# Optimization experiments

Measured on AMD Instinct MI355X. Metric: run time of the kernel, lower is better.

## Reference

```python
import jax, jax.numpy as jnp
import numpy as np

C = 32           # max_channels (in == out == 32, stride 1)
K = 3            # base kernel size
EXP_NITER = 5    # ConvExponential iterations -> effective kernel 11x11
POWER_IT = 3     # FantasticFour power iterations
B, H, W = 16, 256, 256


def _l2n(x):
    # L2Normalize over all dims (applied on store via right_inverse and again on read; idempotent)
    return x / (jnp.sqrt(jnp.sum(x * x)) + 1e-12)


def _skew(k):
    # K - flip(K^T, spatial)
    return k - jnp.flip(jnp.transpose(k, (1, 0, 2, 3)), axis=(2, 3))


def _fantastic_four(kernel, u1, u2, u3, u4):
    u1, u2, u3, u4 = map(_l2n, (u1, u2, u3, u4))
    for _ in range(POWER_IT):
        v1 = _l2n(jnp.sum(kernel * u1, axis=(1, 3), keepdims=True))
        u1 = _l2n(jnp.sum(kernel * v1, axis=(0, 2), keepdims=True))
        v2 = _l2n(jnp.sum(kernel * u2, axis=(1, 2), keepdims=True))
        u2 = _l2n(jnp.sum(kernel * v2, axis=(0, 3), keepdims=True))
        v3 = _l2n(jnp.sum(kernel * u3, axis=(1, 2, 3), keepdims=True))
        u3 = _l2n(jnp.sum(kernel * v3, axis=0, keepdims=True))
        v4 = _l2n(jnp.sum(kernel * u4, axis=(0, 2, 3), keepdims=True))
        u4 = _l2n(jnp.sum(kernel * v4, axis=1, keepdims=True))
    sg = jax.lax.stop_gradient  # sigmas use detached u/v, grad only via kernel
    s1 = jnp.sum(kernel * sg(u1) * sg(v1))
    s2 = jnp.sum(kernel * sg(u2) * sg(v2))
    s3 = jnp.sum(kernel * sg(u3) * sg(v3))
    s4 = jnp.sum(kernel * sg(u4) * sg(v4))
    sigma = jnp.minimum(jnp.minimum(s1, s2), jnp.minimum(s3, s4))
    return kernel / sigma


def _conv_exp(kernel):
    # kernel_global = I + K + K*K/2! + ... (kernel composition = full spatial convolution)
    p = (K - 1) // 2
    ident = jnp.pad(jnp.eye(C, dtype=kernel.dtype)[:, :, None, None],
                    ((0, 0), (0, 0), (p, p), (p, p)))
    kg = kernel + ident            # (C, C, K, K)
    ki = kernel
    rhs = jnp.flip(kernel, axis=(2, 3))  # flip -> lax correlation becomes full convolution
    for i in range(2, EXP_NITER + 1):
        # out[o,d,y,x] = sum_{c,p,q} ki[c,d,y-p,x-q] * kernel[o,c,p,q]
        inp = jnp.transpose(ki, (1, 0, 2, 3))  # (d, c, h, w) as NCHW
        out = jax.lax.conv_general_dilated(
            inp, rhs, window_strides=(1, 1),
            padding=[(K - 1, K - 1), (K - 1, K - 1)],
            dimension_numbers=('NCHW', 'OIHW', 'NCHW'))
        ki = jnp.transpose(out, (1, 0, 2, 3)) / float(i)
        kg = jnp.pad(kg, ((0, 0), (0, 0), (p, p), (p, p))) + ki
    return kg  # (C, C, 11, 11) for K=3, EXP_NITER=5


def reference(x, weight_raw, bias, u1, u2, u3, u4):
    w = _conv_exp(_fantastic_four(_skew(weight_raw), u1, u2, u3, u4))
    pad = w.shape[2] // 2  # 5
    z = jnp.pad(x, ((0, 0), (0, 0), (pad, pad), (pad, pad)), mode='wrap')  # circular
    z = jax.lax.conv_general_dilated(
        z, w, window_strides=(1, 1), padding='VALID',
        dimension_numbers=('NCHW', 'OIHW', 'NCHW'))
    return z + bias[None, :, None, None]


def setup_inputs() -> dict:
    key = jax.random.key(0)
    ks = jax.random.split(key, 7)
    return {
        'x': jax.random.normal(ks[0], (B, C, H, W), dtype=jnp.float32),
        'weight_raw': jax.random.normal(ks[1], (C, C, K, K), dtype=jnp.float32),
        'bias': jax.random.normal(ks[2], (C,), dtype=jnp.float32),
        'u1': jax.random.normal(ks[3], (1, C, 1, K), dtype=jnp.float32),
        'u2': jax.random.normal(ks[4], (1, C, K, 1), dtype=jnp.float32),
        'u3': jax.random.normal(ks[5], (1, C, K, K), dtype=jnp.float32),
        'u4': jax.random.normal(ks[6], (C, 1, K, K), dtype=jnp.float32),
    }
```

## Files before the change

kernel.cpp:

```cpp
#include <hip/hip_runtime.h>
#include <math.h>

typedef __bf16 bf16x8 __attribute__((ext_vector_type(8)));
typedef float f32x16 __attribute__((ext_vector_type(16)));
typedef unsigned int uint4v __attribute__((ext_vector_type(4)));

__device__ __forceinline__ unsigned short bf16_rne(float f) {
    unsigned u = __float_as_uint(f);
    unsigned r = u + 0x7fffu + ((u >> 16) & 1u);
    return (unsigned short)(r >> 16);
}
__device__ __forceinline__ float bf16_to_f(unsigned short h) {
    return __uint_as_float(((unsigned)h) << 16);
}

__device__ __forceinline__ float block_sum256(float v, float* red) {
    #pragma unroll
    for (int off = 32; off > 0; off >>= 1)
        v += __shfl_down(v, off, 64);
    const int tid = threadIdx.x;
    if ((tid & 63) == 0) red[tid >> 6] = v;
    __syncthreads();
    float tot = red[0] + red[1] + red[2] + red[3];
    __syncthreads();
    return tot;
}

__device__ __forceinline__ void l2n_lds(float* a, int n, float* red) {
    float s = 0.f;
    for (int i = threadIdx.x; i < n; i += 256) s += a[i] * a[i];
    const float tot = block_sum256(s, red);
    const float sc = 1.0f / (sqrtf(tot) + 1e-12f);
    for (int i = threadIdx.x; i < n; i += 256) a[i] *= sc;
    __syncthreads();
}

__global__ __launch_bounds__(256) void ff_kernel(
    const float* __restrict__ wr,
    const float* __restrict__ u1g, const float* __restrict__ u2g,
    const float* __restrict__ u3g, const float* __restrict__ u4g,
    float* __restrict__ kf_out)
{
    __shared__ float ks[9216];
    __shared__ float u1[96], v1[96], u2[96], v2[96];
    __shared__ float u3[288], u4[288], v3[32], v4[32];
    __shared__ float red[8];
    const int tid = threadIdx.x;

    for (int i = tid; i < 9216; i += 256) {
        int q  = i % 3;
        int p  = (i / 3) % 3;
        int ic = (i / 9) % 32;
        int oc = i / 288;
        ks[i] = wr[i] - wr[ic * 288 + oc * 9 + (2 - p) * 3 + (2 - q)];
    }
    if (tid < 96) { u1[tid] = u1g[tid]; u2[tid] = u2g[tid]; }
    for (int i = tid; i < 288; i += 256) { u3[i] = u3g[i]; u4[i] = u4g[i]; }
    __syncthreads();
    l2n_lds(u1, 96, red);
    l2n_lds(u2, 96, red);
    l2n_lds(u3, 288, red);
    l2n_lds(u4, 288, red);

    for (int it = 0; it < 3; ++it) {
        if (tid < 96) {
            int o = tid / 3, p = tid % 3;
            float s = 0.f;
            for (int i = 0; i < 32; ++i)
                for (int q = 0; q < 3; ++q)
                    s += ks[o * 288 + i * 9 + p * 3 + q] * u1[i * 3 + q];
            v1[tid] = s;
        }
        __syncthreads();
        l2n_lds(v1, 96, red);
        if (tid < 96) {
            int i = tid / 3, q = tid % 3;
            float s = 0.f;
            for (int o = 0; o < 32; ++o)
                for (int p = 0; p < 3; ++p)
                    s += ks[o * 288 + i * 9 + p * 3 + q] * v1[o * 3 + p];
            u1[tid] = s;
        }
        __syncthreads();
        l2n_lds(u1, 96, red);
        if (tid < 96) {
            int o = tid / 3, q = tid % 3;
            float s = 0.f;
            for (int i = 0; i < 32; ++i)
                for (int p = 0; p < 3; ++p)
                    s += ks[o * 288 + i * 9 + p * 3 + q] * u2[i * 3 + p];
            v2[tid] = s;
        }
        __syncthreads();
        l2n_lds(v2, 96, red);
        if (tid < 96) {
            int i = tid / 3, p = tid % 3;
            float s = 0.f;
            for (int o = 0; o < 32; ++o)
                for (int q = 0; q < 3; ++q)
                    s += ks[o * 288 + i * 9 + p * 3 + q] * v2[o * 3 + q];
            u2[tid] = s;
        }
        __syncthreads();
        l2n_lds(u2, 96, red);
        if (tid < 32) {
            float s = 0.f;
            for (int i = 0; i < 32; ++i)
                for (int pq = 0; pq < 9; ++pq)
                    s += ks[tid * 288 + i * 9 + pq] * u3[i * 9 + pq];
            v3[tid] = s;
        }
        __syncthreads();
        l2n_lds(v3, 32, red);
        for (int j = tid; j < 288; j += 256) {
            float s = 0.f;
            for (int o = 0; o < 32; ++o)
                s += ks[o * 288 + j] * v3[o];
            u3[j] = s;
        }
        __syncthreads();
        l2n_lds(u3, 288, red);
        if (tid < 32) {
            float s = 0.f;
            for (int o = 0; o < 32; ++o)
                for (int pq = 0; pq < 9; ++pq)
                    s += ks[o * 288 + tid * 9 + pq] * u4[o * 9 + pq];
            v4[tid] = s;
        }
        __syncthreads();
        l2n_lds(v4, 32, red);
        for (int j = tid; j < 288; j += 256) {
            int o = j / 9, pq = j - o * 9;
            float s = 0.f;
            for (int i = 0; i < 32; ++i)
                s += ks[o * 288 + i * 9 + pq] * v4[i];
            u4[j] = s;
        }
        __syncthreads();
        l2n_lds(u4, 288, red);
    }

    float p1 = 0.f, p2 = 0.f, p3 = 0.f, p4 = 0.f;
    for (int idx = tid; idx < 9216; idx += 256) {
        int q = idx % 3;
        int p = (idx / 3) % 3;
        int i = (idx / 9) % 32;
        int o = idx / 288;
        float k = ks[idx];
        p1 += k * u1[i * 3 + q] * v1[o * 3 + p];
        p2 += k * u2[i * 3 + p] * v2[o * 3 + q];
        p3 += k * u3[i * 9 + p * 3 + q] * v3[o];
        p4 += k * u4[o * 9 + p * 3 + q] * v4[i];
    }
    float s1 = block_sum256(p1, red);
    float s2 = block_sum256(p2, red);
    float s3 = block_sum256(p3, red);
    float s4 = block_sum256(p4, red);
    float sigma = fminf(fminf(s1, s2), fminf(s3, s4));
    for (int idx = tid; idx < 9216; idx += 256)
        kf_out[idx] = ks[idx] / sigma;
}

__global__ void initacc_kernel(const float* __restrict__ kf, float* __restrict__ wacc) {
    int idx = blockIdx.x * 256 + threadIdx.x;
    if (idx >= 123904) return;
    int o = idx / 3872;
    int rem = idx - o * 3872;
    int c = rem / 121;
    int yx = rem - c * 121;
    int y = yx / 11, x = yx - y * 11;
    float v = (o == c && y == 5 && x == 5) ? 1.0f : 0.0f;
    if (y >= 4 && y <= 6 && x >= 4 && x <= 6)
        v += kf[o * 288 + c * 9 + (y - 4) * 3 + (x - 4)];
    wacc[idx] = v;
}

__global__ void expstep_kernel(const float* __restrict__ kf, const float* __restrict__ ki,
                               float* __restrict__ ko, float* __restrict__ wacc,
                               int S, float scale)
{
    const int S2 = S + 2;
    const int off = (11 - S2) >> 1;
    const int o = blockIdx.x >> 5;
    const int d = blockIdx.x & 31;
    for (int yx = threadIdx.x; yx < S2 * S2; yx += blockDim.x) {
        int y = yx / S2, xx = yx - y * S2;
        float s = 0.f;
        for (int c = 0; c < 32; ++c) {
            const float* kfo = kf + o * 288 + c * 9;
            const float* kic = ki + (c * 32 + d) * S * S;
            #pragma unroll
            for (int p = 0; p < 3; ++p) {
                int yy = y - p;
                if (yy < 0 || yy >= S) continue;
                #pragma unroll
                for (int q = 0; q < 3; ++q) {
                    int xq = xx - q;
                    if (xq < 0 || xq >= S) continue;
                    s += kfo[p * 3 + q] * kic[yy * S + xq];
                }
            }
        }
        s *= scale;
        ko[(o * 32 + d) * S2 * S2 + yx] = s;
        wacc[(o * 32 + d) * 121 + (y + off) * 11 + (xx + off)] += s;
    }
}

__global__ void wprep_kernel(const float* __restrict__ wacc, uint4v* __restrict__ wbuf) {
    int idx = blockIdx.x * 256 + threadIdx.x;
    if (idx >= 30976) return;
    int lane  = idx & 63;
    int split = (idx >> 6) & 1;
    int ch    = (idx >> 7) & 1;
    int tap   = idx >> 8;
    int o     = lane & 31;
    int cbase = ch * 16 + ((lane >> 5) << 3);
    unsigned short v[8];
    #pragma unroll
    for (int j = 0; j < 8; ++j) {
        float w = wacc[o * 3872 + (cbase + j) * 121 + tap];
        unsigned short h = bf16_rne(w);
        v[j] = split ? bf16_rne(w - bf16_to_f(h)) : h;
    }
    uint4v u;
    u.x = (unsigned)v[0] | ((unsigned)v[1] << 16);
    u.y = (unsigned)v[2] | ((unsigned)v[3] << 16);
    u.z = (unsigned)v[4] | ((unsigned)v[5] << 16);
    u.w = (unsigned)v[6] | ((unsigned)v[7] << 16);
    wbuf[idx] = u;
}

__device__ __forceinline__ void pack2(unsigned short* dst, const unsigned short* v) {
    uint4v u;
    u.x = (unsigned)v[0] | ((unsigned)v[1] << 16);
    u.y = (unsigned)v[2] | ((unsigned)v[3] << 16);
    u.z = (unsigned)v[4] | ((unsigned)v[5] << 16);
    u.w = (unsigned)v[6] | ((unsigned)v[7] << 16);
    *(uint4v*)dst = u;
}

template<bool TWOPASS, bool DOSTAGE, bool STHI>
__device__ __forceinline__ void mfma_phase(
    f32x16 (&acc)[4],
    const uint4v* __restrict__ wbuf,
    const uint4v* __restrict__ pb,
    unsigned short* __restrict__ dst,
    int schlf,
    int chlf,
    const float* __restrict__ x,
    int b, int Y0, int X0, int tid, int lane, int ywave, int myoff)
{
    const int wb0 = chlf * 128 + lane;
    #pragma unroll 1
    for (int q = 0; q < 11; ++q) {
        if (DOSTAGE) {
            if (!(q & 1) && (q >> 1) < 5) {
                int pix = tid + ((q >> 1) << 8);
                if (pix < 1092) {
                    int rr = pix / 42, ss = pix - rr * 42;
                    int gy = (Y0 + rr - 5) & 255;
                    int gx = (X0 + ss - 5) & 255;
                    const float* xp = x + (((size_t)(b * 32 + schlf * 16)) << 16)
                                        + (gy << 8) + gx;
                    unsigned short wv[16];
                    #pragma unroll
                    for (int cc = 0; cc < 16; ++cc) {
                        float v = xp[(size_t)cc << 16];
                        unsigned short h = bf16_rne(v);
                        wv[cc] = STHI ? h : bf16_rne(v - bf16_to_f(h));
                    }
                    pack2(&dst[pix * 8], wv);
                    pack2(&dst[(1092 + pix) * 8], wv + 8);
                }
            }
        }
        uint4v ah[8], al[8];
        ah[0] = wbuf[wb0 + q * 256];
        ah[1] = wbuf[wb0 + (11 + q) * 256];
        ah[2] = wbuf[wb0 + (22 + q) * 256];
        if (TWOPASS) {
            al[0] = wbuf[wb0 + q * 256 + 64];
            al[1] = wbuf[wb0 + (11 + q) * 256 + 64];
            al[2] = wbuf[wb0 + (22 + q) * 256 + 64];
        }
        bf16x8 B = __builtin_bit_cast(bf16x8, pb[ywave * 42 + q + myoff]);
        #pragma unroll
        for (int r = 0; r < 14; ++r) {
            const bf16x8 cB = B;
            if (r < 13)
                B = __builtin_bit_cast(bf16x8, pb[(ywave + r + 1) * 42 + q + myoff]);
            if (r + 3 <= 10) {
                ah[(r + 3) & 7] = wbuf[wb0 + ((r + 3) * 11 + q) * 256];
                if (TWOPASS)
                    al[(r + 3) & 7] = wbuf[wb0 + ((r + 3) * 11 + q) * 256 + 64];
            }
            const int plo = (r - 3 > 0) ? r - 3 : 0;
            const int phi = (r < 10) ? r : 10;
            __builtin_amdgcn_s_setprio(1);
            #pragma unroll
            for (int p = plo; p <= phi; ++p)
                acc[r - p] = __builtin_amdgcn_mfma_f32_32x32x16_bf16(
                    __builtin_bit_cast(bf16x8, ah[p & 7]), cB, acc[r - p], 0, 0, 0);
            if (TWOPASS) {
                #pragma unroll
                for (int p = plo; p <= phi; ++p)
                    acc[r - p] = __builtin_amdgcn_mfma_f32_32x32x16_bf16(
                        __builtin_bit_cast(bf16x8, al[p & 7]), cB, acc[r - p], 0, 0, 0);
            }
            __builtin_amdgcn_s_setprio(0);
        }
    }
}

__global__ __launch_bounds__(256, 2) void conv_mfma_kernel(
    const float* __restrict__ x, const uint4v* __restrict__ wbuf,
    const float* __restrict__ bias, float* __restrict__ out)
{
    __shared__ unsigned short bufA[2 * 1092 * 8];
    __shared__ unsigned short bufB[2 * 1092 * 8];
    __shared__ float biasS[32];

    const int b    = blockIdx.z;
    const int Y0   = blockIdx.y << 4;
    const int X0   = blockIdx.x << 5;
    const int tid  = threadIdx.x;
    const int lane = tid & 63;
    const int ywave = (tid >> 6) << 2;
    const int myoff = (lane & 31) + (lane >> 5) * 1092;

    if (tid < 32) biasS[tid] = bias[tid];

    f32x16 acc[4];
    #pragma unroll
    for (int s = 0; s < 4; ++s)
        #pragma unroll
        for (int r = 0; r < 16; ++r) acc[s][r] = 0.f;

    {
        const float* xb = x + (((size_t)(b * 32)) << 16);
        for (int pix = tid; pix < 1092; pix += 256) {
            int r = pix / 42, s = pix - r * 42;
            int gy = (Y0 + r - 5) & 255;
            int gx = (X0 + s - 5) & 255;
            const float* xp = xb + (gy << 8) + gx;
            unsigned short hv[16], lv[16];
            #pragma unroll
            for (int cc = 0; cc < 16; ++cc) {
                float v = xp[(size_t)cc << 16];
                unsigned short h = bf16_rne(v);
                hv[cc] = h;
                lv[cc] = bf16_rne(v - bf16_to_f(h));
            }
            pack2(&bufA[pix * 8], hv);
            pack2(&bufA[(1092 + pix) * 8], hv + 8);
            pack2(&bufB[pix * 8], lv);
            pack2(&bufB[(1092 + pix) * 8], lv + 8);
        }
    }
    __syncthreads();

    mfma_phase<true, false, false>(acc, wbuf, (const uint4v*)bufA, nullptr, 0, 0,
                                   x, b, Y0, X0, tid, lane, ywave, myoff);
    __syncthreads();

    mfma_phase<false, true, true>(acc, wbuf, (const uint4v*)bufB, bufA, 1, 0,
                                  x, b, Y0, X0, tid, lane, ywave, myoff);
    __syncthreads();

    mfma_phase<true, true, false>(acc, wbuf, (const uint4v*)bufA, bufB, 1, 1,
                                  x, b, Y0, X0, tid, lane, ywave, myoff);
    __syncthreads();

    mfma_phase<false, false, false>(acc, wbuf, (const uint4v*)bufB, nullptr, 1, 1,
                                    x, b, Y0, X0, tid, lane, ywave, myoff);

    const int colx = X0 + (lane & 31);
    const int half = lane >> 5;
    #pragma unroll
    for (int s = 0; s < 4; ++s) {
        int y = Y0 + ywave + s;
        #pragma unroll
        for (int r = 0; r < 16; ++r) {
            int o = (r & 3) + ((r >> 2) << 3) + (half << 2);
            out[(((size_t)(b * 32 + o)) << 16) + (y << 8) + colx] = acc[s][r] + biasS[o];
        }
    }
}

extern "C" void kernel_launch(void* const* d_in, const int* in_sizes, int n_in,
                              void* d_out, int out_size, void* d_ws, size_t ws_size,
                              hipStream_t stream) {
    const float* x    = (const float*)d_in[0];
    const float* wraw = (const float*)d_in[1];
    const float* bias = (const float*)d_in[2];
    const float* u1   = (const float*)d_in[3];
    const float* u2   = (const float*)d_in[4];
    const float* u3   = (const float*)d_in[5];
    const float* u4   = (const float*)d_in[6];
    float* out = (float*)d_out;

    float* ws   = (float*)d_ws;
    float* kf   = ws;
    float* bufA = kf + 9216;
    float* bufB = bufA + 123904;
    float* wacc = bufB + 123904;
    uint4v* wbuf = (uint4v*)(wacc + 123904);

    ff_kernel<<<1, 256, 0, stream>>>(wraw, u1, u2, u3, u4, kf);
    initacc_kernel<<<484, 256, 0, stream>>>(kf, wacc);
    expstep_kernel<<<1024, 128, 0, stream>>>(kf, kf,   bufA, wacc, 3, 0.5f);
    expstep_kernel<<<1024, 128, 0, stream>>>(kf, bufA, bufB, wacc, 5, 1.0f / 3.0f);
    expstep_kernel<<<1024, 128, 0, stream>>>(kf, bufB, bufA, wacc, 7, 0.25f);
    expstep_kernel<<<1024, 128, 0, stream>>>(kf, bufA, bufB, wacc, 9, 0.2f);
    wprep_kernel<<<121, 256, 0, stream>>>(wacc, wbuf);

    conv_mfma_kernel<<<dim3(8, 16, 16), 256, 0, stream>>>(x, wbuf, bias, out);
}
```

Baseline: 931.7 us.

## Use single shared buffer with serialized staging to raise occupancy to three blocks

Replaces the two double-buffered shared-memory planes with one buffer. Each hi/lo plane is now staged synchronously before its MFMA pass instead of being overlapped with the previous pass, and launch bounds are raised to 3 blocks per CU. Halving LDS use and capping registers is meant to let more blocks hide latency across CUs. In exchange, global loads are no longer overlapped with MFMA work inside a block, and the tighter register cap could cause spills. Staging is also fully serialized within each block.

```diff
diff --git a/kernel.cpp b/kernel.cpp
--- a/kernel.cpp
+++ b/kernel.cpp
@@ -240,41 +240,38 @@
     *(uint4v*)dst = u;
 }
 
-template<bool TWOPASS, bool DOSTAGE, bool STHI>
-__device__ __forceinline__ void mfma_phase(
+__device__ __forceinline__ void stage_plane(
+    unsigned short* __restrict__ buf, const float* __restrict__ x,
+    int b, int chlf, bool lo, int Y0, int X0, int tid)
+{
+    const float* xb = x + (((size_t)(b * 32 + chlf * 16)) << 16);
+    for (int pix = tid; pix < 1092; pix += 256) {
+        int r = pix / 42, s = pix - r * 42;
+        int gy = (Y0 + r - 5) & 255;
+        int gx = (X0 + s - 5) & 255;
+        const float* xp = xb + (gy << 8) + gx;
+        unsigned short v[16];
+        #pragma unroll
+        for (int cc = 0; cc < 16; ++cc) {
+            float t = xp[(size_t)cc << 16];
+            unsigned short h = bf16_rne(t);
+            v[cc] = lo ? bf16_rne(t - bf16_to_f(h)) : h;
+        }
+        pack2(&buf[pix * 8], v);
+        pack2(&buf[(1092 + pix) * 8], v + 8);
+    }
+}
+
+template<bool TWOPASS>
+__device__ __forceinline__ void mfma_pass(
     f32x16 (&acc)[4],
     const uint4v* __restrict__ wbuf,
     const uint4v* __restrict__ pb,
-    unsigned short* __restrict__ dst,
-    int schlf,
-    int chlf,
-    const float* __restrict__ x,
-    int b, int Y0, int X0, int tid, int lane, int ywave, int myoff)
+    int chlf, int lane, int ywave, int myoff)
 {
     const int wb0 = chlf * 128 + lane;
     #pragma unroll 1
     for (int q = 0; q < 11; ++q) {
-        if (DOSTAGE) {
-            if (!(q & 1) && (q >> 1) < 5) {
-                int pix = tid + ((q >> 1) << 8);
-                if (pix < 1092) {
-                    int rr = pix / 42, ss = pix - rr * 42;
-                    int gy = (Y0 + rr - 5) & 255;
-                    int gx = (X0 + ss - 5) & 255;
-                    const float* xp = x + (((size_t)(b * 32 + schlf * 16)) << 16)
-                                        + (gy << 8) + gx;
-                    unsigned short wv[16];
-                    #pragma unroll
-                    for (int cc = 0; cc < 16; ++cc) {
-                        float v = xp[(size_t)cc << 16];
-                        unsigned short h = bf16_rne(v);
-                        wv[cc] = STHI ? h : bf16_rne(v - bf16_to_f(h));
-                    }
-                    pack2(&dst[pix * 8], wv);
-                    pack2(&dst[(1092 + pix) * 8], wv + 8);
-                }
-            }
-        }
         uint4v ah[8], al[8];
         ah[0] = wbuf[wb0 + q * 256];
         ah[1] = wbuf[wb0 + (11 + q) * 256];
@@ -313,12 +310,11 @@
     }
 }
 
-__global__ __launch_bounds__(256, 2) void conv_mfma_kernel(
+__global__ __launch_bounds__(256, 3) void conv_mfma_kernel(
     const float* __restrict__ x, const uint4v* __restrict__ wbuf,
     const float* __restrict__ bias, float* __restrict__ out)
 {
-    __shared__ unsigned short bufA[2 * 1092 * 8];
-    __shared__ unsigned short bufB[2 * 1092 * 8];
+    __shared__ unsigned short sbuf[2 * 1092 * 8];
     __shared__ float biasS[32];
 
     const int b    = blockIdx.z;
@@ -337,43 +333,19 @@
         #pragma unroll
         for (int r = 0; r < 16; ++r) acc[s][r] = 0.f;
 
-    {
-        const float* xb = x + (((size_t)(b * 32)) << 16);
-        for (int pix = tid; pix < 1092; pix += 256) {
-            int r = pix / 42, s = pix - r * 42;
-            int gy = (Y0 + r - 5) & 255;
-            int gx = (X0 + s - 5) & 255;
-            const float* xp = xb + (gy << 8) + gx;
-            unsigned short hv[16], lv[16];
-            #pragma unroll
-            for (int cc = 0; cc < 16; ++cc) {
-                float v = xp[(size_t)cc << 16];
-                unsigned short h = bf16_rne(v);
-                hv[cc] = h;
-                lv[cc] = bf16_rne(v - bf16_to_f(h));
-            }
-            pack2(&bufA[pix * 8], hv);
-            pack2(&bufA[(1092 + pix) * 8], hv + 8);
-            pack2(&bufB[pix * 8], lv);
-            pack2(&bufB[(1092 + pix) * 8], lv + 8);
-        }
-    }
-    __syncthreads();
-
-    mfma_phase<true, false, false>(acc, wbuf, (const uint4v*)bufA, nullptr, 0, 0,
-                                   x, b, Y0, X0, tid, lane, ywave, myoff);
-    __syncthreads();
-
-    mfma_phase<false, true, true>(acc, wbuf, (const uint4v*)bufB, bufA, 1, 0,
-                                  x, b, Y0, X0, tid, lane, ywave, myoff);
-    __syncthreads();
-
-    mfma_phase<true, true, false>(acc, wbuf, (const uint4v*)bufA, bufB, 1, 1,
-                                  x, b, Y0, X0, tid, lane, ywave, myoff);
-    __syncthreads();
-
-    mfma_phase<false, false, false>(acc, wbuf, (const uint4v*)bufB, nullptr, 1, 1,
-                                    x, b, Y0, X0, tid, lane, ywave, myoff);
+    const uint4v* pb = (const uint4v*)sbuf;
+
+    #pragma unroll 1
+    for (int chlf = 0; chlf < 2; ++chlf) {
+        stage_plane(sbuf, x, b, chlf, false, Y0, X0, tid);
+        __syncthreads();
+        mfma_pass<true>(acc, wbuf, pb, chlf, lane, ywave, myoff);
+        __syncthreads();
+        stage_plane(sbuf, x, b, chlf, true, Y0, X0, tid);
+        __syncthreads();
+        mfma_pass<false>(acc, wbuf, pb, chlf, lane, ywave, myoff);
+        __syncthreads();
+    }
 
     const int colx = X0 + (lane & 31);
     const int half = lane >> 5;
```

Measured after the change: 975.8 us. 1.05x slower.
